# Kernel optimization log

Measured on AMD Instinct MI355X. Metric: run time of the kernel, lower is better.

## Reference

```python
import jax, jax.numpy as jnp
import numpy as np

E, H, HD = 2048, 32, 64
SCALE = HD ** -0.5


def setup_inputs() -> dict:
    key = jax.random.key(0)
    ks = jax.random.split(key, 11)
    B, T, P = 16, 4, 4096
    S = P + T
    return {
        "hidden_states": jax.random.normal(ks[0], (B, T, E), jnp.float32),
        "past_key": jax.random.normal(ks[1], (1, H, P, HD), jnp.float32),
        "past_value": jax.random.normal(ks[2], (1, H, P, HD), jnp.float32),
        "attention_mask": jnp.zeros((B, 1, T, S), jnp.float32),
        "Wq": jax.random.normal(ks[3], (E, E), jnp.float32) * 0.02,
        "bq": jax.random.normal(ks[4], (E,), jnp.float32) * 0.02,
        "Wk": jax.random.normal(ks[5], (E, E), jnp.float32) * 0.02,
        "bk": jax.random.normal(ks[6], (E,), jnp.float32) * 0.02,
        "Wv": jax.random.normal(ks[7], (E, E), jnp.float32) * 0.02,
        "bv": jax.random.normal(ks[8], (E,), jnp.float32) * 0.02,
        "Wo": jax.random.normal(ks[9], (E, E), jnp.float32) * 0.02,
        "bo": jax.random.normal(ks[10], (E,), jnp.float32) * 0.02,
    }


def _shape(x, B, S):
    # [B,S,E] -> [B,H,S,hd]
    return x.reshape(B, S, H, HD).transpose(0, 2, 1, 3)


def reference(hidden_states, past_key, past_value, attention_mask,
              Wq, bq, Wk, bk, Wv, bv, Wo, bo):
    B, T, _ = hidden_states.shape
    # projections (torch Linear: x @ W.T + b); query pre-scaled
    q = _shape(hidden_states @ Wq.T + bq, B, T) * SCALE   # [B,H,T,hd]
    k_new = _shape(hidden_states @ Wk.T + bk, B, T)       # [B,H,T,hd]
    v_new = _shape(hidden_states @ Wv.T + bv, B, T)
    # cache stored with batch 1, broadcast (torch repeat) to B, then concat
    k_past = jnp.broadcast_to(past_key, (B,) + past_key.shape[1:])
    v_past = jnp.broadcast_to(past_value, (B,) + past_value.shape[1:])
    k = jnp.concatenate([k_past, k_new], axis=2)          # [B,H,S,hd]
    v = jnp.concatenate([v_past, v_new], axis=2)
    scores = jnp.einsum('bhtd,bhsd->bhts', q, k)          # [B,H,T,S]
    scores = scores + attention_mask                      # mask is [B,1,T,S]
    scores = jnp.maximum(scores, jnp.finfo(scores.dtype).min)
    w = jax.nn.softmax(scores, axis=-1)
    out = jnp.einsum('bhts,bhsd->bhtd', w, v)             # [B,H,T,hd]
    out = out.transpose(0, 2, 1, 3).reshape(B, T, E)
    return out @ Wo.T + bo
```

## Files before the change

kernel.cpp:

```cpp
#include <hip/hip_runtime.h>


typedef float f4 __attribute__((ext_vector_type(4)));
typedef short s8v __attribute__((ext_vector_type(8)));

#define NEG_HUGE (-3.402823466e38f)

__device__ inline unsigned short f2bs(float x) {
  union { float f; unsigned int u; } a; a.f = x;
  unsigned int u = a.u;
  u += 0x7fffu + ((u >> 16) & 1u);
  return (unsigned short)(u >> 16);
}
__device__ inline float bs2f(unsigned short s) {
  union { unsigned int u; float f; } a; a.u = ((unsigned int)s) << 16;
  return a.f;
}
__device__ inline s8v cvt8(f4 a, f4 b) {
  s8v r;
  r[0]=(short)f2bs(a[0]); r[1]=(short)f2bs(a[1]); r[2]=(short)f2bs(a[2]); r[3]=(short)f2bs(a[3]);
  r[4]=(short)f2bs(b[0]); r[5]=(short)f2bs(b[1]); r[6]=(short)f2bs(b[2]); r[7]=(short)f2bs(b[3]);
  return r;
}
__device__ inline f4 mfma16(s8v a, s8v b, f4 c) {
  return __builtin_amdgcn_mfma_f32_16x16x32_bf16(a, b, c, 0, 0, 0);
}
__device__ inline f4 fzero() { f4 z = {0.f,0.f,0.f,0.f}; return z; }
__device__ inline float wave_sum(float v) {
  #pragma unroll
  for (int off = 32; off; off >>= 1) v += __shfl_xor(v, off, 64);
  return v;
}

__global__ __launch_bounds__(256) void k_hs2bf(
    const float* __restrict__ hs, unsigned short* __restrict__ hsb) {
  const int i = (blockIdx.x * 256 + threadIdx.x) * 8;
  f4 a0 = *reinterpret_cast<const f4*>(hs + i);
  f4 a1 = *reinterpret_cast<const f4*>(hs + i + 4);
  s8v r = cvt8(a0, a1);
  *reinterpret_cast<s8v*>(hsb + i) = r;
}

__global__ __launch_bounds__(512) void k_qkvp(
    const unsigned short* __restrict__ hsb, const float* __restrict__ Wq,
    const float* __restrict__ Wk, const float* __restrict__ Wv,
    const float* __restrict__ bq, const float* __restrict__ bk,
    const float* __restrict__ bv, unsigned short* __restrict__ qws,
    float* __restrict__ knew, float* __restrict__ vnew) {
  __shared__ float red[6][16][17];
  const int n0 = (blockIdx.x >> 1) * 16;
  const int mh = blockIdx.x & 1;
  const int p = n0 >> 11;
  const int c0 = n0 & 2047;
  const float* W = (p == 0) ? Wq : (p == 1) ? Wk : Wv;
  const float* bias = (p == 0) ? bq : (p == 1) ? bk : bv;
  const int t = threadIdx.x, lane = t & 63, w = t >> 6;
  const int mt = w & 1, kq = w >> 1;
  const int cl = lane & 15, q = lane >> 4;
  const int rbase = mh * 32 + mt * 16;

  const unsigned short* arow = hsb + (rbase + cl) * 2048 + kq * 512 + q * 8;
  const float* brow = W + (size_t)(c0 + cl) * 2048 + kq * 512 + q * 8;

  f4 acc = fzero();
  #pragma unroll
  for (int k0 = 0; k0 < 512; k0 += 32) {
    s8v af = *reinterpret_cast<const s8v*>(arow + k0);
    f4 b0 = *reinterpret_cast<const f4*>(brow + k0);
    f4 b1 = *reinterpret_cast<const f4*>(brow + k0 + 4);
    acc = mfma16(af, cvt8(b0, b1), acc);
  }
  if (kq) {
    #pragma unroll
    for (int rg = 0; rg < 4; ++rg) red[(kq - 1) * 2 + mt][q * 4 + rg][cl] = acc[rg];
  }
  __syncthreads();
  if (kq == 0) {
    const int c = c0 + cl, h = c >> 6, d = c & 63;
    #pragma unroll
    for (int rg = 0; rg < 4; ++rg) {
      const int rr = q * 4 + rg;
      const int r = rbase + rr;
      const int b = r >> 2, tt = r & 3;
      float v = acc[rg] + red[mt][rr][cl] + red[2 + mt][rr][cl]
              + red[4 + mt][rr][cl] + bias[c];
      if (p == 0) {
        qws[h * 4608 + r * 72 + d] = f2bs(v * 0.125f);
      } else if (p == 1) {
        knew[((h * 16 + b) * 4 + tt) * 64 + d] = v;
      } else {
        vnew[((h * 16 + b) * 4 + tt) * 64 + d] = v;
      }
    }
  }
}

__global__ __launch_bounds__(256) void k_flash(
    const unsigned short* __restrict__ qws, const float* __restrict__ Kp,
    const float* __restrict__ Vp, const float* __restrict__ mask,
    float* __restrict__ Opart, float* __restrict__ mpart,
    float* __restrict__ lpart) {
  __shared__ __align__(16) unsigned short Pb[64 * 136];
  __shared__ __align__(16) unsigned short Vb[128 * 74];
  __shared__ float s2[256];
  __shared__ float mrow[64];
  __shared__ float psum[4][64];
  float* tmp = reinterpret_cast<float*>(Pb);

  const int bx = blockIdx.x;
  const int h = bx & 31, cch = bx >> 5;
  const int s0 = cch * 128;
  const int t = threadIdx.x, lane = t & 63, w = t >> 6;
  const int cl = lane & 15, q = lane >> 4;
  const float* Kh = Kp + (size_t)h * 4096 * 64;
  const float* Vh = Vp + (size_t)h * 4096 * 64;

  unsigned int* Vb32 = reinterpret_cast<unsigned int*>(Vb);
  #pragma unroll
  for (int i = 0; i < 8; ++i) {
    int idx = t + i * 256;
    int s = idx >> 4, d4 = (idx & 15) << 2;
    f4 v = *reinterpret_cast<const f4*>(Vh + (size_t)(s0 + s) * 64 + d4);
    unsigned int lo = (unsigned int)f2bs(v[0]) | ((unsigned int)f2bs(v[1]) << 16);
    unsigned int hi = (unsigned int)f2bs(v[2]) | ((unsigned int)f2bs(v[3]) << 16);
    int u = s * 37 + (d4 >> 1);
    Vb32[u] = lo; Vb32[u + 1] = hi;
  }

  s8v afr[4][2];
  #pragma unroll
  for (int mt = 0; mt < 4; ++mt)
    #pragma unroll
    for (int k2 = 0; k2 < 2; ++k2)
      afr[mt][k2] = *reinterpret_cast<const s8v*>(
          qws + h * 4608 + (mt * 16 + cl) * 72 + k2 * 32 + q * 8);

  f4 sc[2][4];
  #pragma unroll
  for (int ni = 0; ni < 2; ++ni)
    #pragma unroll
    for (int mt = 0; mt < 4; ++mt) sc[ni][mt] = fzero();
  #pragma unroll
  for (int ni = 0; ni < 2; ++ni) {
    const int srow = s0 + (w * 2 + ni) * 16 + cl;
    const float* kr = Kh + (size_t)srow * 64 + q * 8;
    #pragma unroll
    for (int k2 = 0; k2 < 2; ++k2) {
      f4 k0v = *reinterpret_cast<const f4*>(kr + k2 * 32);
      f4 k1v = *reinterpret_cast<const f4*>(kr + k2 * 32 + 4);
      s8v bf = cvt8(k0v, k1v);
      #pragma unroll
      for (int mt = 0; mt < 4; ++mt)
        sc[ni][mt] = mfma16(afr[mt][k2], bf, sc[ni][mt]);
    }
  }
  #pragma unroll
  for (int mt = 0; mt < 4; ++mt)
    #pragma unroll
    for (int rg = 0; rg < 4; ++rg) {
      const int r = mt * 16 + q * 4 + rg;
      float mx = NEG_HUGE;
      #pragma unroll
      for (int ni = 0; ni < 2; ++ni) {
        const int col = s0 + (w * 2 + ni) * 16 + cl;
        float v = sc[ni][mt][rg] + mask[(size_t)r * 4100 + col];
        v = fmaxf(v, NEG_HUGE);
        sc[ni][mt][rg] = v;
        mx = fmaxf(mx, v);
      }
      tmp[r * 68 + w * 16 + cl] = mx;
    }
  __syncthreads();
  {
    const int row = t >> 2, qt = t & 3;
    const float* tr = tmp + row * 68 + qt * 16;
    float m = fmaxf(fmaxf(tr[0], tr[1]), fmaxf(tr[2], tr[3]));
    #pragma unroll
    for (int j = 4; j < 16; j += 4)
      m = fmaxf(m, fmaxf(fmaxf(tr[j], tr[j+1]), fmaxf(tr[j+2], tr[j+3])));
    s2[row * 4 + qt] = m;
  }
  __syncthreads();
  if (t < 64) {
    float m = fmaxf(fmaxf(s2[t*4], s2[t*4+1]), fmaxf(s2[t*4+2], s2[t*4+3]));
    mrow[t] = m;
    mpart[(h * 32 + cch) * 64 + t] = m;
  }
  __syncthreads();
  #pragma unroll
  for (int mt = 0; mt < 4; ++mt)
    #pragma unroll
    for (int rg = 0; rg < 4; ++rg) {
      const int r = mt * 16 + q * 4 + rg;
      const float m = mrow[r];
      #pragma unroll
      for (int ni = 0; ni < 2; ++ni) {
        float e = __expf(sc[ni][mt][rg] - m);
        Pb[r * 136 + (w * 2 + ni) * 16 + cl] = f2bs(e);
      }
    }
  __syncthreads();
  {
    const int r = t & 63, qt = t >> 6;
    float s = 0.f;
    #pragma unroll
    for (int j8 = 0; j8 < 4; ++j8) {
      const unsigned short* pp = &Pb[r * 136 + qt * 32 + j8 * 8];
      #pragma unroll
      for (int j = 0; j < 8; ++j) s += bs2f(pp[j]);
    }
    psum[qt][r] = s;
  }
  f4 oacc[4];
  #pragma unroll
  for (int mt = 0; mt < 4; ++mt) oacc[mt] = fzero();
  const int dcol = w * 16 + cl;
  #pragma unroll
  for (int k2 = 0; k2 < 4; ++k2) {
    const int sb = k2 * 32 + q * 8;
    s8v bf;
    #pragma unroll
    for (int j = 0; j < 8; ++j) bf[j] = (short)Vb[(sb + j) * 74 + dcol];
    #pragma unroll
    for (int mt = 0; mt < 4; ++mt) {
      s8v pa = *reinterpret_cast<const s8v*>(&Pb[(mt * 16 + cl) * 136 + sb]);
      oacc[mt] = mfma16(pa, bf, oacc[mt]);
    }
  }
  __syncthreads();
  if (t < 64)
    lpart[(h * 32 + cch) * 64 + t] = psum[0][t] + psum[1][t] + psum[2][t] + psum[3][t];
  float* ob = Opart + (size_t)(h * 32 + cch) * 64 * 64;
  #pragma unroll
  for (int mt = 0; mt < 4; ++mt)
    #pragma unroll
    for (int rg = 0; rg < 4; ++rg)
      ob[(mt * 16 + q * 4 + rg) * 64 + dcol] = oacc[mt][rg];
}

__global__ __launch_bounds__(256) void k_merge(
    const unsigned short* __restrict__ qws, const float* __restrict__ knew,
    const float* __restrict__ vnew, const float* __restrict__ mask,
    const float* __restrict__ Opart, const float* __restrict__ mpart,
    const float* __restrict__ lpart, unsigned short* __restrict__ attn) {
  const int bx = blockIdx.x;
  const int h = bx & 31, b = bx >> 5;
  const int d = threadIdx.x & 63, tt = threadIdx.x >> 6;
  const int r = b * 4 + tt;
  float qd = bs2f(qws[h * 4608 + r * 72 + d]);
  float scn[4];
  #pragma unroll
  for (int tp = 0; tp < 4; ++tp) {
    float kn = knew[((h * 16 + b) * 4 + tp) * 64 + d];
    float s = wave_sum(qd * kn);
    s += mask[(size_t)r * 4100 + 4096 + tp];
    scn[tp] = fmaxf(s, NEG_HUGE);
  }
  float mi[32], li[32];
  float mtot = NEG_HUGE;
  #pragma unroll
  for (int i = 0; i < 32; ++i) {
    mi[i] = mpart[(h * 32 + i) * 64 + r];
    li[i] = lpart[(h * 32 + i) * 64 + r];
    mtot = fmaxf(mtot, mi[i]);
  }
  #pragma unroll
  for (int tp = 0; tp < 4; ++tp) mtot = fmaxf(mtot, scn[tp]);
  float ltot = 0.f, od = 0.f;
  #pragma unroll
  for (int i = 0; i < 32; ++i) {
    float fct = __expf(mi[i] - mtot);
    ltot += li[i] * fct;
    od += Opart[((size_t)(h * 32 + i) * 64 + r) * 64 + d] * fct;
  }
  #pragma unroll
  for (int tp = 0; tp < 4; ++tp) {
    float e = __expf(scn[tp] - mtot);
    ltot += e;
    od += e * vnew[((h * 16 + b) * 4 + tp) * 64 + d];
  }
  attn[(size_t)r * 2048 + h * 64 + d] = f2bs(od / ltot);
}

__global__ __launch_bounds__(512) void k_out(
    const unsigned short* __restrict__ attn, const float* __restrict__ Wo,
    const float* __restrict__ bo, float* __restrict__ out) {
  __shared__ float red[6][16][17];
  const int n0 = (blockIdx.x >> 1) * 16;
  const int mh = blockIdx.x & 1;
  const int t = threadIdx.x, lane = t & 63, w = t >> 6;
  const int mt = w & 1, kq = w >> 1;
  const int cl = lane & 15, q = lane >> 4;
  const int rbase = mh * 32 + mt * 16;
  const unsigned short* arow = attn + (size_t)(rbase + cl) * 2048 + kq * 512 + q * 8;
  const float* brow = Wo + (size_t)(n0 + cl) * 2048 + kq * 512 + q * 8;
  f4 acc = fzero();
  #pragma unroll
  for (int k0 = 0; k0 < 512; k0 += 32) {
    s8v af = *reinterpret_cast<const s8v*>(arow + k0);
    f4 b0 = *reinterpret_cast<const f4*>(brow + k0);
    f4 b1 = *reinterpret_cast<const f4*>(brow + k0 + 4);
    acc = mfma16(af, cvt8(b0, b1), acc);
  }
  if (kq) {
    #pragma unroll
    for (int rg = 0; rg < 4; ++rg) red[(kq - 1) * 2 + mt][q * 4 + rg][cl] = acc[rg];
  }
  __syncthreads();
  if (kq == 0) {
    const int c = n0 + cl;
    #pragma unroll
    for (int rg = 0; rg < 4; ++rg) {
      const int rr = q * 4 + rg;
      out[(size_t)(rbase + rr) * 2048 + c] =
          acc[rg] + red[mt][rr][cl] + red[2 + mt][rr][cl] + red[4 + mt][rr][cl] + bo[c];
    }
  }
}

extern "C" void kernel_launch(void* const* d_in, const int* in_sizes, int n_in,
                              void* d_out, int out_size, void* d_ws, size_t ws_size,
                              hipStream_t stream) {
  const float* hs   = (const float*)d_in[0];
  const float* pk   = (const float*)d_in[1];
  const float* pv   = (const float*)d_in[2];
  const float* mask = (const float*)d_in[3];
  const float* Wq   = (const float*)d_in[4];
  const float* bq   = (const float*)d_in[5];
  const float* Wk   = (const float*)d_in[6];
  const float* bk   = (const float*)d_in[7];
  const float* Wv   = (const float*)d_in[8];
  const float* bv   = (const float*)d_in[9];
  const float* Wo   = (const float*)d_in[10];
  const float* bo   = (const float*)d_in[11];

  float* f = (float*)d_ws;
  float* Opart = f;
  float* mpart = Opart + 4194304;
  float* lpart = mpart + 65536;
  float* knew  = lpart + 65536;
  float* vnew  = knew + 131072;
  unsigned short* hsb  = (unsigned short*)(vnew + 131072);
  unsigned short* qws  = hsb + 131072;
  unsigned short* attn = qws + 147456;

  k_hs2bf<<<64, 256, 0, stream>>>(hs, hsb);
  k_qkvp<<<768, 512, 0, stream>>>(hsb, Wq, Wk, Wv, bq, bk, bv, qws, knew, vnew);
  k_flash<<<1024, 256, 0, stream>>>(qws, pk, pv, mask, Opart, mpart, lpart);
  k_merge<<<512, 256, 0, stream>>>(qws, knew, vnew, mask, Opart, mpart, lpart, attn);
  k_out<<<256, 512, 0, stream>>>(attn, Wo, bo, (float*)d_out);
}
```

Baseline: 219.3 us.

## Prefetch GEMM operands, restructure flash reductions, store partials as bf16, widen out-proj

The QKV and output projections now double-buffer their operand loads in registers so memory fetches overlap the MFMAs, and the output projection splits K across 16 waves in 1024-thread blocks. The flash kernel gives each wave one 16-row query tile over all 128 keys, so row max and sum are done with in-wave shuffles instead of several shared-memory passes and barriers. It also issues the V loads before QK so they overlap that compute. Partial outputs are stored as bf16, which halves the merge kernel's traffic but loses some precision. Launch bounds are added to steer register allocation.

```diff
diff --git a/kernel.cpp b/kernel.cpp
--- a/kernel.cpp
+++ b/kernel.cpp
@@ -26,22 +26,16 @@
   return __builtin_amdgcn_mfma_f32_16x16x32_bf16(a, b, c, 0, 0, 0);
 }
 __device__ inline f4 fzero() { f4 z = {0.f,0.f,0.f,0.f}; return z; }
-__device__ inline float wave_sum(float v) {
-  #pragma unroll
-  for (int off = 32; off; off >>= 1) v += __shfl_xor(v, off, 64);
-  return v;
-}
 
 __global__ __launch_bounds__(256) void k_hs2bf(
     const float* __restrict__ hs, unsigned short* __restrict__ hsb) {
   const int i = (blockIdx.x * 256 + threadIdx.x) * 8;
   f4 a0 = *reinterpret_cast<const f4*>(hs + i);
   f4 a1 = *reinterpret_cast<const f4*>(hs + i + 4);
-  s8v r = cvt8(a0, a1);
-  *reinterpret_cast<s8v*>(hsb + i) = r;
-}
-
-__global__ __launch_bounds__(512) void k_qkvp(
+  *reinterpret_cast<s8v*>(hsb + i) = cvt8(a0, a1);
+}
+
+__global__ __launch_bounds__(512, 4) void k_qkvp(
     const unsigned short* __restrict__ hsb, const float* __restrict__ Wq,
     const float* __restrict__ Wk, const float* __restrict__ Wv,
     const float* __restrict__ bq, const float* __restrict__ bk,
@@ -62,13 +56,32 @@
   const unsigned short* arow = hsb + (rbase + cl) * 2048 + kq * 512 + q * 8;
   const float* brow = W + (size_t)(c0 + cl) * 2048 + kq * 512 + q * 8;
 
+  s8v ab[2][4];
+  f4 bb[2][8];
+  auto loadc = [&](int s, int c) {
+    const unsigned short* ap = arow + c * 128;
+    const float* bp = brow + c * 128;
+    #pragma unroll
+    for (int i = 0; i < 4; ++i) {
+      ab[s][i] = *reinterpret_cast<const s8v*>(ap + i * 32);
+      bb[s][2 * i]     = *reinterpret_cast<const f4*>(bp + i * 32);
+      bb[s][2 * i + 1] = *reinterpret_cast<const f4*>(bp + i * 32 + 4);
+    }
+  };
   f4 acc = fzero();
-  #pragma unroll
-  for (int k0 = 0; k0 < 512; k0 += 32) {
-    s8v af = *reinterpret_cast<const s8v*>(arow + k0);
-    f4 b0 = *reinterpret_cast<const f4*>(brow + k0);
-    f4 b1 = *reinterpret_cast<const f4*>(brow + k0 + 4);
-    acc = mfma16(af, cvt8(b0, b1), acc);
+  loadc(0, 0);
+  loadc(1, 1);
+  #pragma unroll
+  for (int c = 0; c < 4; ++c) {
+    const int s = c & 1;
+    s8v a0 = ab[s][0], a1 = ab[s][1], a2 = ab[s][2], a3 = ab[s][3];
+    f4 b0 = bb[s][0], b1 = bb[s][1], b2 = bb[s][2], b3 = bb[s][3];
+    f4 b4 = bb[s][4], b5 = bb[s][5], b6 = bb[s][6], b7 = bb[s][7];
+    if (c < 2) loadc(s, c + 2);
+    acc = mfma16(a0, cvt8(b0, b1), acc);
+    acc = mfma16(a1, cvt8(b2, b3), acc);
+    acc = mfma16(a2, cvt8(b4, b5), acc);
+    acc = mfma16(a3, cvt8(b6, b7), acc);
   }
   if (kq) {
     #pragma unroll
@@ -95,18 +108,13 @@
   }
 }
 
-__global__ __launch_bounds__(256) void k_flash(
+__global__ __launch_bounds__(256, 4) void k_flash(
     const unsigned short* __restrict__ qws, const float* __restrict__ Kp,
     const float* __restrict__ Vp, const float* __restrict__ mask,
-    float* __restrict__ Opart, float* __restrict__ mpart,
+    unsigned short* __restrict__ Opart, float* __restrict__ mpart,
     float* __restrict__ lpart) {
   __shared__ __align__(16) unsigned short Pb[64 * 136];
   __shared__ __align__(16) unsigned short Vb[128 * 74];
-  __shared__ float s2[256];
-  __shared__ float mrow[64];
-  __shared__ float psum[4][64];
-  float* tmp = reinterpret_cast<float*>(Pb);
-
   const int bx = blockIdx.x;
   const int h = bx & 31, cch = bx >> 5;
   const int s0 = cch * 128;
@@ -115,102 +123,94 @@
   const float* Kh = Kp + (size_t)h * 4096 * 64;
   const float* Vh = Vp + (size_t)h * 4096 * 64;
 
-  unsigned int* Vb32 = reinterpret_cast<unsigned int*>(Vb);
+  f4 vreg[8];
   #pragma unroll
   for (int i = 0; i < 8; ++i) {
     int idx = t + i * 256;
     int s = idx >> 4, d4 = (idx & 15) << 2;
-    f4 v = *reinterpret_cast<const f4*>(Vh + (size_t)(s0 + s) * 64 + d4);
-    unsigned int lo = (unsigned int)f2bs(v[0]) | ((unsigned int)f2bs(v[1]) << 16);
-    unsigned int hi = (unsigned int)f2bs(v[2]) | ((unsigned int)f2bs(v[3]) << 16);
-    int u = s * 37 + (d4 >> 1);
-    Vb32[u] = lo; Vb32[u + 1] = hi;
-  }
-
-  s8v afr[4][2];
-  #pragma unroll
-  for (int mt = 0; mt < 4; ++mt)
-    #pragma unroll
-    for (int k2 = 0; k2 < 2; ++k2)
-      afr[mt][k2] = *reinterpret_cast<const s8v*>(
-          qws + h * 4608 + (mt * 16 + cl) * 72 + k2 * 32 + q * 8);
-
-  f4 sc[2][4];
-  #pragma unroll
-  for (int ni = 0; ni < 2; ++ni)
-    #pragma unroll
-    for (int mt = 0; mt < 4; ++mt) sc[ni][mt] = fzero();
-  #pragma unroll
-  for (int ni = 0; ni < 2; ++ni) {
-    const int srow = s0 + (w * 2 + ni) * 16 + cl;
-    const float* kr = Kh + (size_t)srow * 64 + q * 8;
+    vreg[i] = *reinterpret_cast<const f4*>(Vh + (size_t)(s0 + s) * 64 + d4);
+  }
+
+  s8v afr[2];
+  #pragma unroll
+  for (int k2 = 0; k2 < 2; ++k2)
+    afr[k2] = *reinterpret_cast<const s8v*>(
+        qws + h * 4608 + (w * 16 + cl) * 72 + k2 * 32 + q * 8);
+
+  f4 sc[8];
+  #pragma unroll
+  for (int ni = 0; ni < 8; ++ni) {
+    sc[ni] = fzero();
+    const float* kr = Kh + (size_t)(s0 + ni * 16 + cl) * 64 + q * 8;
     #pragma unroll
     for (int k2 = 0; k2 < 2; ++k2) {
       f4 k0v = *reinterpret_cast<const f4*>(kr + k2 * 32);
       f4 k1v = *reinterpret_cast<const f4*>(kr + k2 * 32 + 4);
-      s8v bf = cvt8(k0v, k1v);
-      #pragma unroll
-      for (int mt = 0; mt < 4; ++mt)
-        sc[ni][mt] = mfma16(afr[mt][k2], bf, sc[ni][mt]);
-    }
-  }
-  #pragma unroll
-  for (int mt = 0; mt < 4; ++mt)
-    #pragma unroll
-    for (int rg = 0; rg < 4; ++rg) {
-      const int r = mt * 16 + q * 4 + rg;
-      float mx = NEG_HUGE;
-      #pragma unroll
-      for (int ni = 0; ni < 2; ++ni) {
-        const int col = s0 + (w * 2 + ni) * 16 + cl;
-        float v = sc[ni][mt][rg] + mask[(size_t)r * 4100 + col];
-        v = fmaxf(v, NEG_HUGE);
-        sc[ni][mt][rg] = v;
-        mx = fmaxf(mx, v);
-      }
-      tmp[r * 68 + w * 16 + cl] = mx;
-    }
+      sc[ni] = mfma16(afr[k2], cvt8(k0v, k1v), sc[ni]);
+    }
+  }
+
+  {
+    unsigned int* Vb32 = reinterpret_cast<unsigned int*>(Vb);
+    #pragma unroll
+    for (int i = 0; i < 8; ++i) {
+      int idx = t + i * 256;
+      int s = idx >> 4, d4 = (idx & 15) << 2;
+      f4 v = vreg[i];
+      unsigned int lo = (unsigned int)f2bs(v[0]) | ((unsigned int)f2bs(v[1]) << 16);
+      unsigned int hi = (unsigned int)f2bs(v[2]) | ((unsigned int)f2bs(v[3]) << 16);
+      int u = s * 37 + (d4 >> 1);
+      Vb32[u] = lo; Vb32[u + 1] = hi;
+    }
+  }
+
+  float mx[4] = {NEG_HUGE, NEG_HUGE, NEG_HUGE, NEG_HUGE};
+  #pragma unroll
+  for (int rg = 0; rg < 4; ++rg) {
+    const int r = w * 16 + q * 4 + rg;
+    #pragma unroll
+    for (int ni = 0; ni < 8; ++ni) {
+      float v = sc[ni][rg] + mask[(size_t)r * 4100 + s0 + ni * 16 + cl];
+      v = fmaxf(v, NEG_HUGE);
+      sc[ni][rg] = v;
+      mx[rg] = fmaxf(mx[rg], v);
+    }
+  }
+  #pragma unroll
+  for (int rg = 0; rg < 4; ++rg) {
+    #pragma unroll
+    for (int off = 1; off < 16; off <<= 1)
+      mx[rg] = fmaxf(mx[rg], __shfl_xor(mx[rg], off, 64));
+  }
+  if (cl == 0) {
+    #pragma unroll
+    for (int rg = 0; rg < 4; ++rg)
+      mpart[(h * 32 + cch) * 64 + w * 16 + q * 4 + rg] = mx[rg];
+  }
+  float sm[4] = {0.f, 0.f, 0.f, 0.f};
+  #pragma unroll
+  for (int rg = 0; rg < 4; ++rg) {
+    const int r = w * 16 + q * 4 + rg;
+    #pragma unroll
+    for (int ni = 0; ni < 8; ++ni) {
+      float e = __expf(sc[ni][rg] - mx[rg]);
+      sm[rg] += e;
+      Pb[r * 136 + ni * 16 + cl] = f2bs(e);
+    }
+  }
+  #pragma unroll
+  for (int rg = 0; rg < 4; ++rg) {
+    #pragma unroll
+    for (int off = 1; off < 16; off <<= 1)
+      sm[rg] += __shfl_xor(sm[rg], off, 64);
+  }
+  if (cl == 0) {
+    #pragma unroll
+    for (int rg = 0; rg < 4; ++rg)
+      lpart[(h * 32 + cch) * 64 + w * 16 + q * 4 + rg] = sm[rg];
+  }
   __syncthreads();
-  {
-    const int row = t >> 2, qt = t & 3;
-    const float* tr = tmp + row * 68 + qt * 16;
-    float m = fmaxf(fmaxf(tr[0], tr[1]), fmaxf(tr[2], tr[3]));
-    #pragma unroll
-    for (int j = 4; j < 16; j += 4)
-      m = fmaxf(m, fmaxf(fmaxf(tr[j], tr[j+1]), fmaxf(tr[j+2], tr[j+3])));
-    s2[row * 4 + qt] = m;
-  }
-  __syncthreads();
-  if (t < 64) {
-    float m = fmaxf(fmaxf(s2[t*4], s2[t*4+1]), fmaxf(s2[t*4+2], s2[t*4+3]));
-    mrow[t] = m;
-    mpart[(h * 32 + cch) * 64 + t] = m;
-  }
-  __syncthreads();
-  #pragma unroll
-  for (int mt = 0; mt < 4; ++mt)
-    #pragma unroll
-    for (int rg = 0; rg < 4; ++rg) {
-      const int r = mt * 16 + q * 4 + rg;
-      const float m = mrow[r];
-      #pragma unroll
-      for (int ni = 0; ni < 2; ++ni) {
-        float e = __expf(sc[ni][mt][rg] - m);
-        Pb[r * 136 + (w * 2 + ni) * 16 + cl] = f2bs(e);
-      }
-    }
-  __syncthreads();
-  {
-    const int r = t & 63, qt = t >> 6;
-    float s = 0.f;
-    #pragma unroll
-    for (int j8 = 0; j8 < 4; ++j8) {
-      const unsigned short* pp = &Pb[r * 136 + qt * 32 + j8 * 8];
-      #pragma unroll
-      for (int j = 0; j < 8; ++j) s += bs2f(pp[j]);
-    }
-    psum[qt][r] = s;
-  }
+
   f4 oacc[4];
   #pragma unroll
   for (int mt = 0; mt < 4; ++mt) oacc[mt] = fzero();
@@ -227,21 +227,18 @@
       oacc[mt] = mfma16(pa, bf, oacc[mt]);
     }
   }
-  __syncthreads();
-  if (t < 64)
-    lpart[(h * 32 + cch) * 64 + t] = psum[0][t] + psum[1][t] + psum[2][t] + psum[3][t];
-  float* ob = Opart + (size_t)(h * 32 + cch) * 64 * 64;
+  unsigned short* ob = Opart + (size_t)(h * 32 + cch) * 4096;
   #pragma unroll
   for (int mt = 0; mt < 4; ++mt)
     #pragma unroll
     for (int rg = 0; rg < 4; ++rg)
-      ob[(mt * 16 + q * 4 + rg) * 64 + dcol] = oacc[mt][rg];
+      ob[(mt * 16 + q * 4 + rg) * 64 + dcol] = f2bs(oacc[mt][rg]);
 }
 
 __global__ __launch_bounds__(256) void k_merge(
     const unsigned short* __restrict__ qws, const float* __restrict__ knew,
     const float* __restrict__ vnew, const float* __restrict__ mask,
-    const float* __restrict__ Opart, const float* __restrict__ mpart,
+    const unsigned short* __restrict__ Opart, const float* __restrict__ mpart,
     const float* __restrict__ lpart, unsigned short* __restrict__ attn) {
   const int bx = blockIdx.x;
   const int h = bx & 31, b = bx >> 5;
@@ -252,7 +249,9 @@
   #pragma unroll
   for (int tp = 0; tp < 4; ++tp) {
     float kn = knew[((h * 16 + b) * 4 + tp) * 64 + d];
-    float s = wave_sum(qd * kn);
+    float s = qd * kn;
+    #pragma unroll
+    for (int off = 32; off; off >>= 1) s += __shfl_xor(s, off, 64);
     s += mask[(size_t)r * 4100 + 4096 + tp];
     scn[tp] = fmaxf(s, NEG_HUGE);
   }
@@ -271,7 +270,7 @@
   for (int i = 0; i < 32; ++i) {
     float fct = __expf(mi[i] - mtot);
     ltot += li[i] * fct;
-    od += Opart[((size_t)(h * 32 + i) * 64 + r) * 64 + d] * fct;
+    od += bs2f(Opart[((size_t)(h * 32 + i) * 64 + r) * 64 + d]) * fct;
   }
   #pragma unroll
   for (int tp = 0; tp < 4; ++tp) {
@@ -282,25 +281,40 @@
   attn[(size_t)r * 2048 + h * 64 + d] = f2bs(od / ltot);
 }
 
-__global__ __launch_bounds__(512) void k_out(
+__global__ __launch_bounds__(1024, 4) void k_out(
     const unsigned short* __restrict__ attn, const float* __restrict__ Wo,
     const float* __restrict__ bo, float* __restrict__ out) {
-  __shared__ float red[6][16][17];
+  __shared__ float red[14][16][17];
   const int n0 = (blockIdx.x >> 1) * 16;
   const int mh = blockIdx.x & 1;
   const int t = threadIdx.x, lane = t & 63, w = t >> 6;
   const int mt = w & 1, kq = w >> 1;
   const int cl = lane & 15, q = lane >> 4;
   const int rbase = mh * 32 + mt * 16;
-  const unsigned short* arow = attn + (size_t)(rbase + cl) * 2048 + kq * 512 + q * 8;
-  const float* brow = Wo + (size_t)(n0 + cl) * 2048 + kq * 512 + q * 8;
+  const unsigned short* arow = attn + (size_t)(rbase + cl) * 2048 + kq * 256 + q * 8;
+  const float* brow = Wo + (size_t)(n0 + cl) * 2048 + kq * 256 + q * 8;
+
+  s8v ab[2][4];
+  f4 bb[2][8];
+  auto loadc = [&](int s, int c) {
+    const unsigned short* ap = arow + c * 128;
+    const float* bp = brow + c * 128;
+    #pragma unroll
+    for (int i = 0; i < 4; ++i) {
+      ab[s][i] = *reinterpret_cast<const s8v*>(ap + i * 32);
+      bb[s][2 * i]     = *reinterpret_cast<const f4*>(bp + i * 32);
+      bb[s][2 * i + 1] = *reinterpret_cast<const f4*>(bp + i * 32 + 4);
+    }
+  };
   f4 acc = fzero();
-  #pragma unroll
-  for (int k0 = 0; k0 < 512; k0 += 32) {
-    s8v af = *reinterpret_cast<const s8v*>(arow + k0);
-    f4 b0 = *reinterpret_cast<const f4*>(brow + k0);
-    f4 b1 = *reinterpret_cast<const f4*>(brow + k0 + 4);
-    acc = mfma16(af, cvt8(b0, b1), acc);
+  loadc(0, 0);
+  loadc(1, 1);
+  #pragma unroll
+  for (int c = 0; c < 2; ++c) {
+    const int s = c & 1;
+    #pragma unroll
+    for (int i = 0; i < 4; ++i)
+      acc = mfma16(ab[s][i], cvt8(bb[s][2 * i], bb[s][2 * i + 1]), acc);
   }
   if (kq) {
     #pragma unroll
@@ -312,8 +326,10 @@
     #pragma unroll
     for (int rg = 0; rg < 4; ++rg) {
       const int rr = q * 4 + rg;
-      out[(size_t)(rbase + rr) * 2048 + c] =
-          acc[rg] + red[mt][rr][cl] + red[2 + mt][rr][cl] + red[4 + mt][rr][cl] + bo[c];
+      float v = acc[rg] + bo[c];
+      #pragma unroll
+      for (int j = 0; j < 7; ++j) v += red[j * 2 + mt][rr][cl];
+      out[(size_t)(rbase + rr) * 2048 + c] = v;
     }
   }
 }
@@ -335,12 +351,12 @@
   const float* bo   = (const float*)d_in[11];
 
   float* f = (float*)d_ws;
-  float* Opart = f;
-  float* mpart = Opart + 4194304;
+  float* mpart = f;
   float* lpart = mpart + 65536;
   float* knew  = lpart + 65536;
   float* vnew  = knew + 131072;
-  unsigned short* hsb  = (unsigned short*)(vnew + 131072);
+  unsigned short* Opart = (unsigned short*)(vnew + 131072);
+  unsigned short* hsb  = Opart + 4194304;
   unsigned short* qws  = hsb + 131072;
   unsigned short* attn = qws + 147456;
 
@@ -348,5 +364,5 @@
   k_qkvp<<<768, 512, 0, stream>>>(hsb, Wq, Wk, Wv, bq, bk, bv, qws, knew, vnew);
   k_flash<<<1024, 256, 0, stream>>>(qws, pk, pv, mask, Opart, mpart, lpart);
   k_merge<<<512, 256, 0, stream>>>(qws, knew, vnew, mask, Opart, mpart, lpart, attn);
-  k_out<<<256, 512, 0, stream>>>(attn, Wo, bo, (float*)d_out);
-}
+  k_out<<<256, 1024, 0, stream>>>(attn, Wo, bo, (float*)d_out);
+}
```

Result: slower. 225.6 us (+2.8%).
